# Kernel optimization log

Measured on AMD Instinct MI355X. Metric: run time of the kernel, lower is better.

## Reference

```python
import jax, jax.numpy as jnp
import numpy as np
import math

B, C, H, W = 2, 512, 64, 64
NUM_HEADS = 8
D_K = C // NUM_HEADS
SCALE = 1.0 / math.sqrt(D_K)


def setup_inputs() -> dict:
    key = jax.random.key(0)
    ks = jax.random.split(key, 7)
    init = 0.02
    return {
        "x": jax.random.normal(ks[0], (B, C, H, W), dtype=jnp.float32),
        "Wq": jax.random.normal(ks[1], (C, C), dtype=jnp.float32) * init,
        "bq": jnp.zeros((C,), dtype=jnp.float32),
        "Wkv": jax.random.normal(ks[2], (2 * C, C), dtype=jnp.float32) * init,
        "bkv": jnp.zeros((2 * C,), dtype=jnp.float32),
        "Wp": jax.random.normal(ks[3], (C, C), dtype=jnp.float32) * init,
        "bp": jnp.zeros((C,), dtype=jnp.float32),
    }


def _conv1x1(x, w, b):
    # x: [b, c_in, h, w], w: [c_out, c_in] (1x1 conv kernel), b: [c_out]
    return jnp.einsum('bchw,oc->bohw', x, w) + b[None, :, None, None]


def reference(x, Wq, bq, Wkv, bkv, Wp, bp):
    b, c, h, w = x.shape
    l = h * w
    q = _conv1x1(x, Wq, bq)
    kv = _conv1x1(x, Wkv, bkv)
    k, v = jnp.split(kv, 2, axis=1)
    # reshape to [b, heads, d_k, l]
    q = q.reshape(b, NUM_HEADS, D_K, l)
    k = k.reshape(b, NUM_HEADS, D_K, l)
    v = v.reshape(b, NUM_HEADS, D_K, l)
    attn = jnp.einsum('bhct,bhcs->bhts', q, k) * SCALE  # [b,h,l,l]
    attn = jax.nn.softmax(attn, axis=-1)
    out = jnp.einsum('bhts,bhcs->bhct', attn, v)  # [b,h,d_k,l]
    out = out.reshape(b, c, h, w)
    out = _conv1x1(out, Wp, bp)
    return out
```

## Files before the change

### kernel.cpp

```cpp
#include <hip/hip_runtime.h>
#include <math.h>

#define L_SEQ 4096
#define C_DIM 512
#define NH 8
#define DK 64
#define NB 2
#define QSC 0.18033688011112042f

typedef _Float16 f16;
typedef _Float16 f16x8 __attribute__((ext_vector_type(8)));
typedef _Float16 f16x4 __attribute__((ext_vector_type(4)));
typedef __fp16 h16x2 __attribute__((ext_vector_type(2)));
typedef float f32x4 __attribute__((ext_vector_type(4)));
typedef float f32x16 __attribute__((ext_vector_type(16)));
typedef unsigned int u32;

__global__ __launch_bounds__(256) void prep(
    const float* __restrict__ X, const float* __restrict__ Wq,
    const float* __restrict__ Wkv, const float* __restrict__ Wp,
    f16* __restrict__ Xt, f16* __restrict__ Wqkh,
    f16* __restrict__ Wvh, f16* __restrict__ Wph)
{
    const int tid = threadIdx.x;
    const int z = blockIdx.z;
    if (z < 2) {
        __shared__ f16 Ts[64][72];
        const float* src = X + (size_t)z * C_DIM * L_SEQ;
        f16* dst = Xt + (size_t)z * L_SEQ * C_DIM;
        for (int tile = blockIdx.x; tile < 512; tile += gridDim.x) {
            const int c0 = (tile & 7) * 64;
            const int t0 = (tile >> 3) * 64;
            __syncthreads();
            #pragma unroll
            for (int p = 0; p < 4; ++p) {
                const int c = (tid >> 4) + p * 16;
                const int t = (tid & 15) * 4;
                const float4 v = *(const float4*)(src + (size_t)(c0 + c) * L_SEQ + t0 + t);
                Ts[t + 0][c] = (f16)v.x; Ts[t + 1][c] = (f16)v.y;
                Ts[t + 2][c] = (f16)v.z; Ts[t + 3][c] = (f16)v.w;
            }
            __syncthreads();
            #pragma unroll
            for (int p = 0; p < 2; ++p) {
                const int t = (tid >> 3) + p * 32;
                const int ch = (tid & 7) * 8;
                *(f16x8*)(dst + (size_t)(t0 + t) * C_DIM + c0 + ch) =
                    *(const f16x8*)&Ts[t][ch];
            }
        }
    } else {
        const float* srcs[4] = {Wq, Wkv, Wkv + 262144, Wp};
        f16* dsts[4] = {Wqkh, Wqkh + 262144, Wvh, Wph};
        #pragma unroll
        for (int s = 0; s < 4; ++s) {
            const float* sp = srcs[s]; f16* dp = dsts[s];
            for (int i = blockIdx.x * 256 + tid; i < 65536; i += gridDim.x * 256) {
                const float4 v = *(const float4*)(sp + (size_t)i * 4);
                f16x4 h; h[0] = (f16)v.x; h[1] = (f16)v.y; h[2] = (f16)v.z; h[3] = (f16)v.w;
                *(f16x4*)(dp + (size_t)i * 4) = h;
            }
        }
    }
}

__global__ __launch_bounds__(256) void qk_mfma(
    const f16* __restrict__ Xt, const f16* __restrict__ Wqkh,
    const float* __restrict__ bq, const float* __restrict__ bkv,
    f16* __restrict__ Qh, f16* __restrict__ Kh)
{
    __shared__ f16 As[128][40];
    __shared__ f16 Bs[128][40];
    const int tid = threadIdx.x;
    const int lane = tid & 63, w = tid >> 6;
    const int l15 = lane & 15, quad = lane >> 4;
    const int wy = w >> 1, wx = w & 1;
    const int mb0 = blockIdx.x * 128;
    const int n0  = blockIdx.y * 128;

    f32x4 acc[4][4] = {};
    const int row = tid >> 2, c8 = (tid & 3) * 8;
    const f16* aptr = Xt + (size_t)mb0 * 512;
    const f16* bptr = Wqkh + (size_t)n0 * 512;

    uint4 ga0 = *(const uint4*)(aptr + (size_t)row * 512 + c8);
    uint4 ga1 = *(const uint4*)(aptr + (size_t)(row + 64) * 512 + c8);
    uint4 gb0 = *(const uint4*)(bptr + (size_t)row * 512 + c8);
    uint4 gb1 = *(const uint4*)(bptr + (size_t)(row + 64) * 512 + c8);

    for (int k0 = 0; k0 < 512; k0 += 32) {
        __syncthreads();
        *(uint4*)&As[row][c8] = ga0;
        *(uint4*)&As[row + 64][c8] = ga1;
        *(uint4*)&Bs[row][c8] = gb0;
        *(uint4*)&Bs[row + 64][c8] = gb1;
        if (k0 + 32 < 512) {
            ga0 = *(const uint4*)(aptr + (size_t)row * 512 + k0 + 32 + c8);
            ga1 = *(const uint4*)(aptr + (size_t)(row + 64) * 512 + k0 + 32 + c8);
            gb0 = *(const uint4*)(bptr + (size_t)row * 512 + k0 + 32 + c8);
            gb1 = *(const uint4*)(bptr + (size_t)(row + 64) * 512 + k0 + 32 + c8);
        }
        __syncthreads();
        f16x8 af[4], bf[4];
        #pragma unroll
        for (int i = 0; i < 4; ++i)
            af[i] = *(const f16x8*)&As[wy * 64 + i * 16 + l15][quad * 8];
        #pragma unroll
        for (int n = 0; n < 4; ++n)
            bf[n] = *(const f16x8*)&Bs[wx * 64 + n * 16 + l15][quad * 8];
        #pragma unroll
        for (int i = 0; i < 4; ++i)
            #pragma unroll
            for (int n = 0; n < 4; ++n)
                acc[i][n] = __builtin_amdgcn_mfma_f32_16x16x32_f16(af[i], bf[n], acc[i][n], 0, 0, 0);
    }

    #pragma unroll
    for (int nn = 0; nn < 4; ++nn) {
        const int o = n0 + wx * 64 + nn * 16 + l15;
        const bool isQ = (o < 512);
        const float bias = isQ ? bq[o] : bkv[o - 512];
        const int h = (o & 511) >> 6, d = o & 63;
        f16* base = isQ ? Qh : Kh;
        #pragma unroll
        for (int i = 0; i < 4; ++i) {
            const int tr = mb0 + wy * 64 + i * 16 + quad * 4;
            #pragma unroll
            for (int r = 0; r < 4; ++r) {
                const int tg = tr + r;
                const int bh = (tg >> 12) * NH + h;
                float v = acc[i][nn][r] + bias;
                if (isQ) v *= QSC;
                base[((size_t)bh * L_SEQ + (tg & 4095)) * DK + d] = (f16)v;
            }
        }
    }
}

__global__ __launch_bounds__(256) void cproj_mfma(
    const f16* __restrict__ Bsrc, const f16* __restrict__ Wh,
    const float* __restrict__ bias, f16* __restrict__ outV,
    float* __restrict__ outP, int mode)
{
    __shared__ f16 As[128][40];
    __shared__ f16 Bs[128][40];
    const int tid = threadIdx.x;
    const int lane = tid & 63, w = tid >> 6;
    const int l15 = lane & 15, quad = lane >> 4;
    const int wy = w >> 1, wx = w & 1;
    const int n0  = blockIdx.x * 128;
    const int mb0 = blockIdx.y * 128;

    f32x4 acc[4][4] = {};
    const int row = tid >> 2, c8 = (tid & 3) * 8;
    const f16* aptr = Wh + (size_t)mb0 * 512;
    const f16* bptr = Bsrc + (size_t)n0 * 512;

    uint4 ga0 = *(const uint4*)(aptr + (size_t)row * 512 + c8);
    uint4 ga1 = *(const uint4*)(aptr + (size_t)(row + 64) * 512 + c8);
    uint4 gb0 = *(const uint4*)(bptr + (size_t)row * 512 + c8);
    uint4 gb1 = *(const uint4*)(bptr + (size_t)(row + 64) * 512 + c8);

    for (int k0 = 0; k0 < 512; k0 += 32) {
        __syncthreads();
        *(uint4*)&As[row][c8] = ga0;
        *(uint4*)&As[row + 64][c8] = ga1;
        *(uint4*)&Bs[row][c8] = gb0;
        *(uint4*)&Bs[row + 64][c8] = gb1;
        if (k0 + 32 < 512) {
            ga0 = *(const uint4*)(aptr + (size_t)row * 512 + k0 + 32 + c8);
            ga1 = *(const uint4*)(aptr + (size_t)(row + 64) * 512 + k0 + 32 + c8);
            gb0 = *(const uint4*)(bptr + (size_t)row * 512 + k0 + 32 + c8);
            gb1 = *(const uint4*)(bptr + (size_t)(row + 64) * 512 + k0 + 32 + c8);
        }
        __syncthreads();
        f16x8 af[4], bf[4];
        #pragma unroll
        for (int i = 0; i < 4; ++i)
            af[i] = *(const f16x8*)&As[wy * 64 + i * 16 + l15][quad * 8];
        #pragma unroll
        for (int n = 0; n < 4; ++n)
            bf[n] = *(const f16x8*)&Bs[wx * 64 + n * 16 + l15][quad * 8];
        #pragma unroll
        for (int i = 0; i < 4; ++i)
            #pragma unroll
            for (int n = 0; n < 4; ++n)
                acc[i][n] = __builtin_amdgcn_mfma_f32_16x16x32_f16(af[i], bf[n], acc[i][n], 0, 0, 0);
    }

    const int l15p = (l15 & 3) | ((l15 & 4) << 1) | ((l15 & 8) >> 1);

    #pragma unroll
    for (int i = 0; i < 4; ++i) {
        #pragma unroll
        for (int r = 0; r < 4; ++r) {
            const int o = mb0 + wy * 64 + i * 16 + quad * 4 + r;
            const float bv = bias[o];
            #pragma unroll
            for (int nn = 0; nn < 4; ++nn) {
                const int tg = n0 + wx * 64 + nn * 16 + l15;
                const float v = acc[i][nn][r] + bv;
                if (mode == 0) {
                    const int tgp = (tg & ~15) | l15p;
                    const int bh = (tgp >> 12) * NH + (o >> 6);
                    outV[((size_t)bh * DK + (o & 63)) * L_SEQ + (tgp & 4095)] = (f16)v;
                } else {
                    outP[((size_t)(tg >> 12) * C_DIM + o) * L_SEQ + (tg & 4095)] = v;
                }
            }
        }
    }
}

__device__ __forceinline__ void gload_lds16(const char* g, char* l) {
    __builtin_amdgcn_global_load_lds(
        (const __attribute__((address_space(1))) void*)g,
        (__attribute__((address_space(3))) void*)l, 16, 0, 0);
}

__global__ __launch_bounds__(256, 2) void flash16(
    const f16* __restrict__ Qh, const f16* __restrict__ Kh,
    const f16* __restrict__ Vh, f16* __restrict__ Opart,
    float* __restrict__ Lpart)
{
    __shared__ f16 KS[2][64 * 64];
    __shared__ f16 VS[2][64 * 64];
    const int tid = threadIdx.x;
    const int lane = tid & 63, w = tid >> 6;
    const int l31 = lane & 31, hl = lane >> 5;
    const int bh = blockIdx.x;
    const int t0 = blockIdx.y * 256;
    const int half = blockIdx.z;
    const int s_beg = half * 2048, s_end = s_beg + 2048;
    const int wtb = t0 + w * 64;
    const f16* Qg = Qh + (size_t)bh * L_SEQ * DK;
    const char* Kg = (const char*)(Kh + (size_t)bh * L_SEQ * DK);
    const char* Vg = (const char*)(Vh + (size_t)bh * DK * L_SEQ);

    f16x8 qf0[4], qf1[4];
    #pragma unroll
    for (int kst = 0; kst < 4; ++kst) {
        qf0[kst] = *(const f16x8*)(Qg + (size_t)(wtb + l31) * DK + kst * 16 + hl * 8);
        qf1[kst] = *(const f16x8*)(Qg + (size_t)(wtb + 32 + l31) * DK + kst * 16 + hl * 8);
    }

    const int c0 = tid, c1 = tid + 256;
    const int kofs0 = (c0 >> 3) * 128  + (((c0 & 7) * 16) ^ (((c0 >> 3) & 7) << 4));
    const int kofs1 = (c1 >> 3) * 128  + (((c1 & 7) * 16) ^ (((c1 >> 3) & 7) << 4));
    const int vofs0 = (c0 >> 3) * 8192 + (((c0 & 7) * 16) ^ (((c0 >> 3) & 7) << 4));
    const int vofs1 = (c1 >> 3) * 8192 + (((c1 & 7) * 16) ^ (((c1 >> 3) & 7) << 4));
    const int lb0 = (w * 64) * 16, lb1 = (256 + w * 64) * 16;

    #define STAGE(bufi, s0v) do {                                   \
        const char* kg_ = Kg + (size_t)(s0v) * 128;                 \
        const char* vg_ = Vg + (size_t)(s0v) * 2;                   \
        char* kl_ = (char*)&KS[bufi][0];                            \
        char* vl_ = (char*)&VS[bufi][0];                            \
        gload_lds16(kg_ + kofs0, kl_ + lb0);                        \
        gload_lds16(kg_ + kofs1, kl_ + lb1);                        \
        gload_lds16(vg_ + vofs0, vl_ + lb0);                        \
        gload_lds16(vg_ + vofs1, vl_ + lb1);                        \
    } while (0)

    f32x16 O00 = {}, O01 = {}, O10 = {}, O11 = {};
    float rs0 = 0.f, rs1 = 0.f;
    h16x2 one2; one2[0] = (__fp16)1.f; one2[1] = (__fp16)1.f;

    STAGE(0, s_beg);
    __syncthreads();

    const int swz = (l31 & 7) << 4;
    const int rowA = l31 * 128, rowB = (32 + l31) * 128;

    int cur = 0;
    for (int s0 = s_beg; s0 < s_end; s0 += 64) {
        if (s0 + 64 < s_end) STAGE(cur ^ 1, s0 + 64);

        const char* Kb = (const char*)&KS[cur][0];
        const char* Vb = (const char*)&VS[cur][0];

        f32x16 Sa0 = {}, Sa1 = {}, Sb0 = {}, Sb1 = {};
        __builtin_amdgcn_s_setprio(1);
        #pragma unroll
        for (int kst = 0; kst < 4; ++kst) {
            const int cb = (kst * 32 + hl * 16) ^ swz;
            const f16x8 k0 = *(const f16x8*)(Kb + rowA + cb);
            const f16x8 k1 = *(const f16x8*)(Kb + rowB + cb);
            Sa0 = __builtin_amdgcn_mfma_f32_32x32x16_f16(k0, qf0[kst], Sa0, 0, 0, 0);
            Sa1 = __builtin_amdgcn_mfma_f32_32x32x16_f16(k0, qf1[kst], Sa1, 0, 0, 0);
            Sb0 = __builtin_amdgcn_mfma_f32_32x32x16_f16(k1, qf0[kst], Sb0, 0, 0, 0);
            Sb1 = __builtin_amdgcn_mfma_f32_32x32x16_f16(k1, qf1[kst], Sb1, 0, 0, 0);
        }
        __builtin_amdgcn_s_setprio(0);

        union FR { u32 u[4]; f16x8 v; } fr0[4], fr1[4];
        #pragma unroll
        for (int q = 0; q < 4; ++q) {
            const h16x2 a01 = __builtin_amdgcn_cvt_pkrtz(
                __builtin_amdgcn_exp2f(Sa0[4 * q + 0]),
                __builtin_amdgcn_exp2f(Sa0[4 * q + 1]));
            const h16x2 a23 = __builtin_amdgcn_cvt_pkrtz(
                __builtin_amdgcn_exp2f(Sa0[4 * q + 2]),
                __builtin_amdgcn_exp2f(Sa0[4 * q + 3]));
            rs0 = __builtin_amdgcn_fdot2(a01, one2, rs0, false);
            rs0 = __builtin_amdgcn_fdot2(a23, one2, rs0, false);
            union { h16x2 h; u32 u; } p0, p1; p0.h = a01; p1.h = a23;
            fr0[q >> 1].u[(q & 1) * 2 + 0] = p0.u;
            fr0[q >> 1].u[(q & 1) * 2 + 1] = p1.u;
        }
        #pragma unroll
        for (int q = 0; q < 4; ++q) {
            const h16x2 a01 = __builtin_amdgcn_cvt_pkrtz(
                __builtin_amdgcn_exp2f(Sb0[4 * q + 0]),
                __builtin_amdgcn_exp2f(Sb0[4 * q + 1]));
            const h16x2 a23 = __builtin_amdgcn_cvt_pkrtz(
                __builtin_amdgcn_exp2f(Sb0[4 * q + 2]),
                __builtin_amdgcn_exp2f(Sb0[4 * q + 3]));
            rs0 = __builtin_amdgcn_fdot2(a01, one2, rs0, false);
            rs0 = __builtin_amdgcn_fdot2(a23, one2, rs0, false);
            union { h16x2 h; u32 u; } p0, p1; p0.h = a01; p1.h = a23;
            fr0[2 + (q >> 1)].u[(q & 1) * 2 + 0] = p0.u;
            fr0[2 + (q >> 1)].u[(q & 1) * 2 + 1] = p1.u;
        }
        #pragma unroll
        for (int q = 0; q < 4; ++q) {
            const h16x2 a01 = __builtin_amdgcn_cvt_pkrtz(
                __builtin_amdgcn_exp2f(Sa1[4 * q + 0]),
                __builtin_amdgcn_exp2f(Sa1[4 * q + 1]));
            const h16x2 a23 = __builtin_amdgcn_cvt_pkrtz(
                __builtin_amdgcn_exp2f(Sa1[4 * q + 2]),
                __builtin_amdgcn_exp2f(Sa1[4 * q + 3]));
            rs1 = __builtin_amdgcn_fdot2(a01, one2, rs1, false);
            rs1 = __builtin_amdgcn_fdot2(a23, one2, rs1, false);
            union { h16x2 h; u32 u; } p0, p1; p0.h = a01; p1.h = a23;
            fr1[q >> 1].u[(q & 1) * 2 + 0] = p0.u;
            fr1[q >> 1].u[(q & 1) * 2 + 1] = p1.u;
        }
        #pragma unroll
        for (int q = 0; q < 4; ++q) {
            const h16x2 a01 = __builtin_amdgcn_cvt_pkrtz(
                __builtin_amdgcn_exp2f(Sb1[4 * q + 0]),
                __builtin_amdgcn_exp2f(Sb1[4 * q + 1]));
            const h16x2 a23 = __builtin_amdgcn_cvt_pkrtz(
                __builtin_amdgcn_exp2f(Sb1[4 * q + 2]),
                __builtin_amdgcn_exp2f(Sb1[4 * q + 3]));
            rs1 = __builtin_amdgcn_fdot2(a01, one2, rs1, false);
            rs1 = __builtin_amdgcn_fdot2(a23, one2, rs1, false);
            union { h16x2 h; u32 u; } p0, p1; p0.h = a01; p1.h = a23;
            fr1[2 + (q >> 1)].u[(q & 1) * 2 + 0] = p0.u;
            fr1[2 + (q >> 1)].u[(q & 1) * 2 + 1] = p1.u;
        }

        __builtin_amdgcn_s_setprio(1);
        #pragma unroll
        for (int kst = 0; kst < 4; ++kst) {
            const int ca = (kst * 32 + hl * 16) ^ swz;
            const f16x8 v0 = *(const f16x8*)(Vb + rowA + ca);
            const f16x8 v1 = *(const f16x8*)(Vb + rowB + ca);
            O00 = __builtin_amdgcn_mfma_f32_32x32x16_f16(v0, fr0[kst].v, O00, 0, 0, 0);
            O01 = __builtin_amdgcn_mfma_f32_32x32x16_f16(v0, fr1[kst].v, O01, 0, 0, 0);
            O10 = __builtin_amdgcn_mfma_f32_32x32x16_f16(v1, fr0[kst].v, O10, 0, 0, 0);
            O11 = __builtin_amdgcn_mfma_f32_32x32x16_f16(v1, fr1[kst].v, O11, 0, 0, 0);
        }
        __builtin_amdgcn_s_setprio(0);

        __syncthreads();
        cur ^= 1;
    }
    #undef STAGE

    rs0 += __shfl_xor(rs0, 32, 64);
    rs1 += __shfl_xor(rs1, 32, 64);
    if (lane < 32) {
        float* Lp = Lpart + (size_t)(half * 16 + bh) * L_SEQ + wtb;
        Lp[l31] = rs0;
        Lp[32 + l31] = rs1;
    }

    f16* Op = Opart + (size_t)(half * 16 + bh) * DK * L_SEQ;
    #pragma unroll
    for (int r = 0; r < 16; ++r) {
        const int d = (r & 3) + 8 * (r >> 2) + 4 * hl;
        Op[(size_t)d * L_SEQ + wtb + l31] = (f16)O00[r];
        Op[(size_t)d * L_SEQ + wtb + 32 + l31] = (f16)O01[r];
        Op[(size_t)(32 + d) * L_SEQ + wtb + l31] = (f16)O10[r];
        Op[(size_t)(32 + d) * L_SEQ + wtb + 32 + l31] = (f16)O11[r];
    }
}

__global__ __launch_bounds__(256) void combine(
    const f16* __restrict__ Opart, const float* __restrict__ Lpart,
    f16* __restrict__ Oh)
{
    __shared__ f16 Ts[64][72];
    __shared__ float Linv[64];
    const int tid = threadIdx.x;
    const int bh = blockIdx.y, b = bh >> 3, h = bh & 7;
    const int t0 = blockIdx.x * 64;
    if (tid < 64) {
        const float lo = Lpart[(size_t)bh * L_SEQ + t0 + tid];
        const float hi = Lpart[(size_t)(16 + bh) * L_SEQ + t0 + tid];
        Linv[tid] = 1.f / (lo + hi);
    }
    __syncthreads();
    const f16* Plo = Opart + (size_t)bh * DK * L_SEQ;
    const f16* Phi = Opart + (size_t)(16 + bh) * DK * L_SEQ;
    const int d = tid >> 4;
    const int tt = (tid & 15) * 4;
    #pragma unroll
    for (int p = 0; p < 4; ++p) {
        const int dd = d + p * 16;
        const size_t off = (size_t)dd * L_SEQ + t0 + tt;
        const f16x4 lo = *(const f16x4*)(Plo + off);
        const f16x4 hi = *(const f16x4*)(Phi + off);
        #pragma unroll
        for (int j = 0; j < 4; ++j)
            Ts[tt + j][dd] = (f16)(((float)lo[j] + (float)hi[j]) * Linv[tt + j]);
    }
    __syncthreads();
    const int tr = tid >> 2, ch = (tid & 3) * 16;
    f16* dst = Oh + ((size_t)(b * L_SEQ + t0 + tr)) * C_DIM + h * DK + ch;
    *(f16x8*)dst = *(const f16x8*)&Ts[tr][ch];
    *(f16x8*)(dst + 8) = *(const f16x8*)&Ts[tr][ch + 8];
}

extern "C" void kernel_launch(void* const* d_in, const int* in_sizes, int n_in,
                              void* d_out, int out_size, void* d_ws, size_t ws_size,
                              hipStream_t stream) {
    (void)in_sizes; (void)n_in; (void)out_size; (void)ws_size;
    const float* x   = (const float*)d_in[0];
    const float* Wq  = (const float*)d_in[1];
    const float* bq  = (const float*)d_in[2];
    const float* Wkv = (const float*)d_in[3];
    const float* bkv = (const float*)d_in[4];
    const float* Wp  = (const float*)d_in[5];
    const float* bp  = (const float*)d_in[6];
    float* out = (float*)d_out;

    f16* Xt    = (f16*)d_ws;
    f16* Wqkh  = Xt + 4194304;
    f16* Wvh   = Wqkh + 524288;
    f16* Wph   = Wvh + 262144;
    f16* Qh    = Wph + 262144;
    f16* Kh    = Qh + 4194304;
    f16* Vh    = Kh + 4194304;
    f16* Oh    = Vh + 4194304;
    f16* Opart = Oh + 4194304;
    float* Lpart = (float*)(Opart + 8388608);

    prep<<<dim3(128, 1, 3), 256, 0, stream>>>(x, Wq, Wkv, Wp, Xt, Wqkh, Wvh, Wph);
    qk_mfma<<<dim3(64, 8), 256, 0, stream>>>(Xt, Wqkh, bq, bkv, Qh, Kh);
    cproj_mfma<<<dim3(64, 4), 256, 0, stream>>>(Xt, Wvh, bkv + 512, Vh, nullptr, 0);
    flash16<<<dim3(16, 16, 2), 256, 0, stream>>>(Qh, Kh, Vh, Opart, Lpart);
    combine<<<dim3(64, 16), 256, 0, stream>>>(Opart, Lpart, Oh);
    cproj_mfma<<<dim3(64, 4), 256, 0, stream>>>(Oh, Wph, bp, nullptr, out, 1);
}
```

Baseline: 205.3 us.

## Software-pipeline QK and PV across iterations with triple-buffered V tiles

```diff
diff --git a/kernel.cpp b/kernel.cpp
--- a/kernel.cpp
+++ b/kernel.cpp
@@ -218,20 +218,40 @@
         (__attribute__((address_space(3))) void*)l, 16, 0, 0);
 }
 
+union FR { u32 u[4]; f16x8 v; };
+
+__device__ __forceinline__ void smax8(const f32x16& S, FR* fr, int base,
+                                      float& rsv, h16x2 one2) {
+    #pragma unroll
+    for (int q = 0; q < 4; ++q) {
+        const h16x2 a01 = __builtin_amdgcn_cvt_pkrtz(
+            __builtin_amdgcn_exp2f(S[4 * q + 0]),
+            __builtin_amdgcn_exp2f(S[4 * q + 1]));
+        const h16x2 a23 = __builtin_amdgcn_cvt_pkrtz(
+            __builtin_amdgcn_exp2f(S[4 * q + 2]),
+            __builtin_amdgcn_exp2f(S[4 * q + 3]));
+        rsv = __builtin_amdgcn_fdot2(a01, one2, rsv, false);
+        rsv = __builtin_amdgcn_fdot2(a23, one2, rsv, false);
+        union { h16x2 h; u32 u; } p0, p1; p0.h = a01; p1.h = a23;
+        fr[base + (q >> 1)].u[(q & 1) * 2 + 0] = p0.u;
+        fr[base + (q >> 1)].u[(q & 1) * 2 + 1] = p1.u;
+    }
+}
+
 __global__ __launch_bounds__(256, 2) void flash16(
     const f16* __restrict__ Qh, const f16* __restrict__ Kh,
     const f16* __restrict__ Vh, f16* __restrict__ Opart,
     float* __restrict__ Lpart)
 {
-    __shared__ f16 KS[2][64 * 64];
-    __shared__ f16 VS[2][64 * 64];
+    __shared__ f16 KS[2][4096];
+    __shared__ f16 VS[3][4096];
     const int tid = threadIdx.x;
     const int lane = tid & 63, w = tid >> 6;
     const int l31 = lane & 31, hl = lane >> 5;
     const int bh = blockIdx.x;
     const int t0 = blockIdx.y * 256;
     const int half = blockIdx.z;
-    const int s_beg = half * 2048, s_end = s_beg + 2048;
+    const int s_beg = half * 2048;
     const int wtb = t0 + w * 64;
     const f16* Qg = Qh + (size_t)bh * L_SEQ * DK;
     const char* Kg = (const char*)(Kh + (size_t)bh * L_SEQ * DK);
@@ -251,123 +271,112 @@
     const int vofs1 = (c1 >> 3) * 8192 + (((c1 & 7) * 16) ^ (((c1 >> 3) & 7) << 4));
     const int lb0 = (w * 64) * 16, lb1 = (256 + w * 64) * 16;
 
-    #define STAGE(bufi, s0v) do {                                   \
-        const char* kg_ = Kg + (size_t)(s0v) * 128;                 \
-        const char* vg_ = Vg + (size_t)(s0v) * 2;                   \
-        char* kl_ = (char*)&KS[bufi][0];                            \
-        char* vl_ = (char*)&VS[bufi][0];                            \
-        gload_lds16(kg_ + kofs0, kl_ + lb0);                        \
-        gload_lds16(kg_ + kofs1, kl_ + lb1);                        \
-        gload_lds16(vg_ + vofs0, vl_ + lb0);                        \
-        gload_lds16(vg_ + vofs1, vl_ + lb1);                        \
+    #define STAGE_K(kb, s0v) do {                                    \
+        const char* kg_ = Kg + (size_t)(s0v) * 128;                  \
+        char* kl_ = (char*)&KS[kb][0];                               \
+        gload_lds16(kg_ + kofs0, kl_ + lb0);                         \
+        gload_lds16(kg_ + kofs1, kl_ + lb1);                         \
+    } while (0)
+    #define STAGE_V(vOfs, s0v) do {                                  \
+        const char* vg_ = Vg + (size_t)(s0v) * 2;                    \
+        char* vl_ = (char*)&VS[0][0] + (vOfs);                       \
+        gload_lds16(vg_ + vofs0, vl_ + lb0);                         \
+        gload_lds16(vg_ + vofs1, vl_ + lb1);                         \
     } while (0)
 
     f32x16 O00 = {}, O01 = {}, O10 = {}, O11 = {};
     float rs0 = 0.f, rs1 = 0.f;
     h16x2 one2; one2[0] = (__fp16)1.f; one2[1] = (__fp16)1.f;
-
-    STAGE(0, s_beg);
+    FR frA0[4], frA1[4], frB0[4], frB1[4];
+
+    STAGE_K(0, s_beg); STAGE_V(0, s_beg);
     __syncthreads();
 
     const int swz = (l31 & 7) << 4;
     const int rowA = l31 * 128, rowB = (32 + l31) * 128;
 
-    int cur = 0;
-    for (int s0 = s_beg; s0 < s_end; s0 += 64) {
-        if (s0 + 64 < s_end) STAGE(cur ^ 1, s0 + 64);
-
-        const char* Kb = (const char*)&KS[cur][0];
-        const char* Vb = (const char*)&VS[cur][0];
-
-        f32x16 Sa0 = {}, Sa1 = {}, Sb0 = {}, Sb1 = {};
-        __builtin_amdgcn_s_setprio(1);
-        #pragma unroll
-        for (int kst = 0; kst < 4; ++kst) {
-            const int cb = (kst * 32 + hl * 16) ^ swz;
-            const f16x8 k0 = *(const f16x8*)(Kb + rowA + cb);
-            const f16x8 k1 = *(const f16x8*)(Kb + rowB + cb);
-            Sa0 = __builtin_amdgcn_mfma_f32_32x32x16_f16(k0, qf0[kst], Sa0, 0, 0, 0);
-            Sa1 = __builtin_amdgcn_mfma_f32_32x32x16_f16(k0, qf1[kst], Sa1, 0, 0, 0);
-            Sb0 = __builtin_amdgcn_mfma_f32_32x32x16_f16(k1, qf0[kst], Sb0, 0, 0, 0);
-            Sb1 = __builtin_amdgcn_mfma_f32_32x32x16_f16(k1, qf1[kst], Sb1, 0, 0, 0);
-        }
-        __builtin_amdgcn_s_setprio(0);
-
-        union FR { u32 u[4]; f16x8 v; } fr0[4], fr1[4];
-        #pragma unroll
-        for (int q = 0; q < 4; ++q) {
-            const h16x2 a01 = __builtin_amdgcn_cvt_pkrtz(
-                __builtin_amdgcn_exp2f(Sa0[4 * q + 0]),
-                __builtin_amdgcn_exp2f(Sa0[4 * q + 1]));
-            const h16x2 a23 = __builtin_amdgcn_cvt_pkrtz(
-                __builtin_amdgcn_exp2f(Sa0[4 * q + 2]),
-                __builtin_amdgcn_exp2f(Sa0[4 * q + 3]));
-            rs0 = __builtin_amdgcn_fdot2(a01, one2, rs0, false);
-            rs0 = __builtin_amdgcn_fdot2(a23, one2, rs0, false);
-            union { h16x2 h; u32 u; } p0, p1; p0.h = a01; p1.h = a23;
-            fr0[q >> 1].u[(q & 1) * 2 + 0] = p0.u;
-            fr0[q >> 1].u[(q & 1) * 2 + 1] = p1.u;
-        }
-        #pragma unroll
-        for (int q = 0; q < 4; ++q) {
-            const h16x2 a01 = __builtin_amdgcn_cvt_pkrtz(
-                __builtin_amdgcn_exp2f(Sb0[4 * q + 0]),
-                __builtin_amdgcn_exp2f(Sb0[4 * q + 1]));
-            const h16x2 a23 = __builtin_amdgcn_cvt_pkrtz(
-                __builtin_amdgcn_exp2f(Sb0[4 * q + 2]),
-                __builtin_amdgcn_exp2f(Sb0[4 * q + 3]));
-            rs0 = __builtin_amdgcn_fdot2(a01, one2, rs0, false);
-            rs0 = __builtin_amdgcn_fdot2(a23, one2, rs0, false);
-            union { h16x2 h; u32 u; } p0, p1; p0.h = a01; p1.h = a23;
-            fr0[2 + (q >> 1)].u[(q & 1) * 2 + 0] = p0.u;
-            fr0[2 + (q >> 1)].u[(q & 1) * 2 + 1] = p1.u;
-        }
-        #pragma unroll
-        for (int q = 0; q < 4; ++q) {
-            const h16x2 a01 = __builtin_amdgcn_cvt_pkrtz(
-                __builtin_amdgcn_exp2f(Sa1[4 * q + 0]),
-                __builtin_amdgcn_exp2f(Sa1[4 * q + 1]));
-            const h16x2 a23 = __builtin_amdgcn_cvt_pkrtz(
-                __builtin_amdgcn_exp2f(Sa1[4 * q + 2]),
-                __builtin_amdgcn_exp2f(Sa1[4 * q + 3]));
-            rs1 = __builtin_amdgcn_fdot2(a01, one2, rs1, false);
-            rs1 = __builtin_amdgcn_fdot2(a23, one2, rs1, false);
-            union { h16x2 h; u32 u; } p0, p1; p0.h = a01; p1.h = a23;
-            fr1[q >> 1].u[(q & 1) * 2 + 0] = p0.u;
-            fr1[q >> 1].u[(q & 1) * 2 + 1] = p1.u;
-        }
-        #pragma unroll
-        for (int q = 0; q < 4; ++q) {
-            const h16x2 a01 = __builtin_amdgcn_cvt_pkrtz(
-                __builtin_amdgcn_exp2f(Sb1[4 * q + 0]),
-                __builtin_amdgcn_exp2f(Sb1[4 * q + 1]));
-            const h16x2 a23 = __builtin_amdgcn_cvt_pkrtz(
-                __builtin_amdgcn_exp2f(Sb1[4 * q + 2]),
-                __builtin_amdgcn_exp2f(Sb1[4 * q + 3]));
-            rs1 = __builtin_amdgcn_fdot2(a01, one2, rs1, false);
-            rs1 = __builtin_amdgcn_fdot2(a23, one2, rs1, false);
-            union { h16x2 h; u32 u; } p0, p1; p0.h = a01; p1.h = a23;
-            fr1[2 + (q >> 1)].u[(q & 1) * 2 + 0] = p0.u;
-            fr1[2 + (q >> 1)].u[(q & 1) * 2 + 1] = p1.u;
-        }
-
+    #define QKBODY(s0v, kbR, kbS, DOSTG, DOPV, stO, pvO, frC0, frC1, frP0, frP1) do { \
+        if (DOSTG) { STAGE_K(kbS, (s0v) + 64); STAGE_V(stO, (s0v) + 64); }  \
+        const char* Kb = (const char*)&KS[kbR][0];                          \
+        f16x8 kf[4];                                                        \
+        _Pragma("unroll")                                                   \
+        for (int kst = 0; kst < 4; ++kst)                                   \
+            kf[kst] = *(const f16x8*)(Kb + rowA + ((kst * 32 + hl * 16) ^ swz)); \
+        {                                                                   \
+            f32x16 Sa0 = {}, Sa1 = {};                                      \
+            __builtin_amdgcn_s_setprio(1);                                  \
+            _Pragma("unroll")                                               \
+            for (int kst = 0; kst < 4; ++kst) {                             \
+                Sa0 = __builtin_amdgcn_mfma_f32_32x32x16_f16(kf[kst], qf0[kst], Sa0, 0, 0, 0); \
+                Sa1 = __builtin_amdgcn_mfma_f32_32x32x16_f16(kf[kst], qf1[kst], Sa1, 0, 0, 0); \
+            }                                                               \
+            __builtin_amdgcn_s_setprio(0);                                  \
+            _Pragma("unroll")                                               \
+            for (int kst = 0; kst < 4; ++kst)                               \
+                kf[kst] = *(const f16x8*)(Kb + rowB + ((kst * 32 + hl * 16) ^ swz)); \
+            smax8(Sa0, frC0, 0, rs0, one2);                                 \
+            smax8(Sa1, frC1, 0, rs1, one2);                                 \
+        }                                                                   \
+        __builtin_amdgcn_sched_barrier(0);                                  \
+        {                                                                   \
+            f32x16 Sb0 = {}, Sb1 = {};                                      \
+            __builtin_amdgcn_s_setprio(1);                                  \
+            _Pragma("unroll")                                               \
+            for (int kst = 0; kst < 4; ++kst) {                             \
+                Sb0 = __builtin_amdgcn_mfma_f32_32x32x16_f16(kf[kst], qf0[kst], Sb0, 0, 0, 0); \
+                Sb1 = __builtin_amdgcn_mfma_f32_32x32x16_f16(kf[kst], qf1[kst], Sb1, 0, 0, 0); \
+            }                                                               \
+            if (DOPV) {                                                     \
+                const char* Vb = (const char*)&VS[0][0] + (pvO);            \
+                _Pragma("unroll")                                           \
+                for (int kst = 0; kst < 4; ++kst) {                         \
+                    const int ca = (kst * 32 + hl * 16) ^ swz;              \
+                    const f16x8 v0 = *(const f16x8*)(Vb + rowA + ca);       \
+                    const f16x8 v1 = *(const f16x8*)(Vb + rowB + ca);       \
+                    O00 = __builtin_amdgcn_mfma_f32_32x32x16_f16(v0, frP0[kst].v, O00, 0, 0, 0); \
+                    O01 = __builtin_amdgcn_mfma_f32_32x32x16_f16(v0, frP1[kst].v, O01, 0, 0, 0); \
+                    O10 = __builtin_amdgcn_mfma_f32_32x32x16_f16(v1, frP0[kst].v, O10, 0, 0, 0); \
+                    O11 = __builtin_amdgcn_mfma_f32_32x32x16_f16(v1, frP1[kst].v, O11, 0, 0, 0); \
+                }                                                           \
+            }                                                               \
+            __builtin_amdgcn_s_setprio(0);                                  \
+            smax8(Sb0, frC0, 2, rs0, one2);                                 \
+            smax8(Sb1, frC1, 2, rs1, one2);                                 \
+        }                                                                   \
+        __syncthreads();                                                    \
+    } while (0)
+
+    QKBODY(s_beg, 0, 1, true, false, 8192, 0, frA0, frA1, frB0, frB1);
+
+    int s0 = s_beg + 64;
+    int stO = 16384, pvO = 0;
+    #pragma unroll 1
+    for (int p = 0; p < 15; ++p) {
+        QKBODY(s0, 1, 0, true, true, stO, pvO, frB0, frB1, frA0, frA1);
+        s0 += 64; stO = (stO == 16384) ? 0 : stO + 8192; pvO = (pvO == 16384) ? 0 : pvO + 8192;
+        QKBODY(s0, 0, 1, true, true, stO, pvO, frA0, frA1, frB0, frB1);
+        s0 += 64; stO = (stO == 16384) ? 0 : stO + 8192; pvO = (pvO == 16384) ? 0 : pvO + 8192;
+    }
+    QKBODY(s0, 1, 0, false, true, 0, pvO, frB0, frB1, frA0, frA1);
+
+    {
+        const char* Vb = (const char*)&VS[0][0] + 8192;
         __builtin_amdgcn_s_setprio(1);
         #pragma unroll
         for (int kst = 0; kst < 4; ++kst) {
             const int ca = (kst * 32 + hl * 16) ^ swz;
             const f16x8 v0 = *(const f16x8*)(Vb + rowA + ca);
             const f16x8 v1 = *(const f16x8*)(Vb + rowB + ca);
-            O00 = __builtin_amdgcn_mfma_f32_32x32x16_f16(v0, fr0[kst].v, O00, 0, 0, 0);
-            O01 = __builtin_amdgcn_mfma_f32_32x32x16_f16(v0, fr1[kst].v, O01, 0, 0, 0);
-            O10 = __builtin_amdgcn_mfma_f32_32x32x16_f16(v1, fr0[kst].v, O10, 0, 0, 0);
-            O11 = __builtin_amdgcn_mfma_f32_32x32x16_f16(v1, fr1[kst].v, O11, 0, 0, 0);
+            O00 = __builtin_amdgcn_mfma_f32_32x32x16_f16(v0, frB0[kst].v, O00, 0, 0, 0);
+            O01 = __builtin_amdgcn_mfma_f32_32x32x16_f16(v0, frB1[kst].v, O01, 0, 0, 0);
+            O10 = __builtin_amdgcn_mfma_f32_32x32x16_f16(v1, frB0[kst].v, O10, 0, 0, 0);
+            O11 = __builtin_amdgcn_mfma_f32_32x32x16_f16(v1, frB1[kst].v, O11, 0, 0, 0);
         }
         __builtin_amdgcn_s_setprio(0);
-
-        __syncthreads();
-        cur ^= 1;
-    }
-    #undef STAGE
+    }
+    #undef QKBODY
+    #undef STAGE_K
+    #undef STAGE_V
 
     rs0 += __shfl_xor(rs0, 32, 64);
     rs1 += __shfl_xor(rs1, 32, 64);
```

After: 203.4 us. Within noise of the previous version (-0.9%).
